# Optimization experiments

Measured on AMD Instinct MI355X. Metric: run time of the kernel, lower is better.

Reference implementation:

```python
import jax, jax.numpy as jnp
import numpy as np

D_G, D_2D, D_3D = 512, 768, 1024
D_F, RANK, ATTN_H = 256, 16, 512
B = 8192


def _xavier(key, shape):
    fan_out, fan_in = shape
    lim = float(np.sqrt(6.0 / (fan_in + fan_out)))
    return jax.random.uniform(key, shape, jnp.float32, -lim, lim)


def setup_inputs() -> dict:
    key = jax.random.key(0)
    ks = jax.random.split(key, 12)
    inp = {
        "h_g": jax.random.normal(ks[0], (B, D_G), jnp.float32),
        "h_2d": jax.random.normal(ks[1], (B, D_2D), jnp.float32),
        "h_3d": jax.random.normal(ks[2], (B, D_3D), jnp.float32),
        # modality projections (torch Linear: y = x @ W.T + b)
        "Wg": _xavier(ks[3], (D_F, D_G)),   "bg": jnp.zeros((D_F,), jnp.float32),
        "W2": _xavier(ks[4], (D_F, D_2D)),  "b2": jnp.zeros((D_F,), jnp.float32),
        "W3": _xavier(ks[5], (D_F, D_3D)),  "b3": jnp.zeros((D_F,), jnp.float32),
        # LayerNorm affine params
        "ln_g_w": jnp.ones((D_F,), jnp.float32),  "ln_g_b": jnp.zeros((D_F,), jnp.float32),
        "ln_2_w": jnp.ones((D_F,), jnp.float32),  "ln_2_b": jnp.zeros((D_F,), jnp.float32),
        "ln_3_w": jnp.ones((D_F,), jnp.float32),  "ln_3_b": jnp.zeros((D_F,), jnp.float32),
        # rank expansions (no bias)
        "U": _xavier(ks[6], (RANK * D_F, D_F)),
        "V": _xavier(ks[7], (RANK * D_F, D_F)),
        "S": _xavier(ks[8], (RANK * D_F, D_F)),
        # attention MLP
        "Wa1": _xavier(ks[9], (ATTN_H, D_G + D_2D + D_3D)), "ba1": jnp.zeros((ATTN_H,), jnp.float32),
        "Wa2": _xavier(ks[10], (RANK, ATTN_H)),             "ba2": jnp.zeros((RANK,), jnp.float32),
    }
    return inp


def _layernorm(x, w, b, eps=1e-5):
    mu = jnp.mean(x, axis=-1, keepdims=True)
    var = jnp.var(x, axis=-1, keepdims=True)
    return (x - mu) * jax.lax.rsqrt(var + eps) * w + b


def reference(h_g, h_2d, h_3d, Wg, bg, W2, b2, W3, b3,
              ln_g_w, ln_g_b, ln_2_w, ln_2_b, ln_3_w, ln_3_b,
              U, V, S, Wa1, ba1, Wa2, ba2):
    # proj + LN + ReLU (dropout=0 / eval mode)
    g = jax.nn.relu(_layernorm(h_g @ Wg.T + bg, ln_g_w, ln_g_b))
    d2 = jax.nn.relu(_layernorm(h_2d @ W2.T + b2, ln_2_w, ln_2_b))
    d3 = jax.nn.relu(_layernorm(h_3d @ W3.T + b3, ln_3_w, ln_3_b))
    b = g.shape[0]
    # rank expansion: (B, R, d_f)
    g_r = (g @ U.T).reshape(b, RANK, D_F)
    d2_r = (d2 @ V.T).reshape(b, RANK, D_F)
    d3_r = (d3 @ S.T).reshape(b, RANK, D_F)
    z_r = g_r * d2_r * d3_r  # elementwise tri-linear product
    # rank attention from raw modality concat
    h_cat = jnp.concatenate([h_g, h_2d, h_3d], axis=-1)
    beta = jax.nn.softmax(jax.nn.relu(h_cat @ Wa1.T + ba1) @ Wa2.T + ba2, axis=-1)  # (B, R)
    z = jnp.einsum('brd,br->bd', z_r, beta)  # (B, d_f)
    return z
```

## Files before the change

### kernel.cpp

```cpp
#include <hip/hip_runtime.h>
#include <stdint.h>

#define B_ROWS 8192
#define DG 512
#define D2 768
#define D3 1024
#define DCAT 2304
#define DF 256
#define RANK 16
#define AH 512

#define OFF_WG 0
#define OFF_W2 131072
#define OFF_W3 327680
#define OFF_U  589824
#define OFF_V  1638400
#define OFF_S  2686976
#define OFF_WA1 3735552

#define WS_WBUF  0u
#define WS_HG    9830400u
#define WS_H2    18219008u
#define WS_H3    30801920u
#define WS_GBUF  47579136u
#define WS_A1P   60162048u
#define WS_ZPART 60162048u
#define WS_BETA  93716480u
#define WS_REQUIRED 94240768u

typedef __attribute__((ext_vector_type(8))) short short8;
typedef __attribute__((ext_vector_type(4))) float f32x4;

__device__ inline unsigned short f2bf(float f) {
  union { float f; unsigned int u; } v; v.f = f;
  unsigned int u = v.u + 0x7fffu + ((v.u >> 16) & 1u);
  return (unsigned short)(u >> 16);
}
__device__ inline float bf2f(unsigned short h) {
  union { float f; unsigned int u; } v; v.u = ((unsigned int)h) << 16;
  return v.f;
}

typedef const unsigned int __attribute__((address_space(1)))* as1_u32p;
typedef unsigned int __attribute__((address_space(3)))* as3_u32p;

__device__ inline void g2l16(const unsigned short* g, unsigned short* l) {
  __builtin_amdgcn_global_load_lds((as1_u32p)g, (as3_u32p)l, 16, 0, 0);
}


__global__ __launch_bounds__(256) void cvt_split_k(const float* __restrict__ hg,
                                                   const float* __restrict__ h2,
                                                   const float* __restrict__ h3,
                                                   const float* __restrict__ Wg,
                                                   const float* __restrict__ W2,
                                                   const float* __restrict__ W3,
                                                   const float* __restrict__ U,
                                                   const float* __restrict__ V,
                                                   const float* __restrict__ S,
                                                   const float* __restrict__ Wa1,
                                                   unsigned short* __restrict__ hgb,
                                                   unsigned short* __restrict__ h2b,
                                                   unsigned short* __restrict__ h3b,
                                                   unsigned short* __restrict__ wbuf) {
  const int bid = blockIdx.x;
  const float* src;
  unsigned short* dst;
  int e;
  if (bid < 18432) {
    e = (bid * 256 + threadIdx.x) * 4;
    if (e < 4194304)        { src = hg + e;            dst = hgb + e; }
    else if (e < 10485760)  { src = h2 + (e - 4194304); dst = h2b + (e - 4194304); }
    else                    { src = h3 + (e - 10485760); dst = h3b + (e - 10485760); }
  } else {
    e = ((bid - 18432) * 256 + threadIdx.x) * 4;
    dst = wbuf + e;
    if (e < OFF_W2)       src = Wg  + e;
    else if (e < OFF_W3)  src = W2  + (e - OFF_W2);
    else if (e < OFF_U)   src = W3  + (e - OFF_W3);
    else if (e < OFF_V)   src = U   + (e - OFF_U);
    else if (e < OFF_S)   src = V   + (e - OFF_V);
    else if (e < OFF_WA1) src = S   + (e - OFF_S);
    else                  src = Wa1 + (e - OFF_WA1);
  }
  float4 v = *(const float4*)src;
  ushort4 o;
  o.x = f2bf(v.x); o.y = f2bf(v.y); o.z = f2bf(v.z); o.w = f2bf(v.w);
  *(ushort4*)dst = o;
}


__global__ __launch_bounds__(512, 2) void fatgemm256_k(const unsigned short* __restrict__ hgb,
                                                       const unsigned short* __restrict__ h2b,
                                                       const unsigned short* __restrict__ h3b,
                                                       const unsigned short* __restrict__ wbuf,
                                                       const float* __restrict__ bg,
                                                       const float* __restrict__ b2,
                                                       const float* __restrict__ b3,
                                                       const float* __restrict__ wg,
                                                       const float* __restrict__ wbg,
                                                       const float* __restrict__ w2,
                                                       const float* __restrict__ wb2,
                                                       const float* __restrict__ w3,
                                                       const float* __restrict__ wb3,
                                                       unsigned short* __restrict__ gout,
                                                       unsigned short* __restrict__ a1part) {
  __shared__ __align__(16) unsigned short lA[2 * 256 * 64];
  __shared__ __align__(16) unsigned short lB[2 * 256 * 64];
  const int bid = blockIdx.x;
  const int tid = threadIdx.x;
  const int lane = tid & 63;
  const int wid = tid >> 6;
  const int wr = wid >> 2;
  const int wc = wid & 3;
  const int row_s = tid >> 3;
  const int kc_s = (((tid & 7) ^ (row_s & 7)) << 3);
  const int mbase = wr * 128 + (lane & 15);
  const int nbase = wc * 64 + (lane & 15);
  const int kq = lane >> 4;
  const int h = lane & 7;

  int role_a1 = 0, half = 0, m0 = 0, n0 = 0, z = 0, nt = 0;
  if (bid < 64)       { role_a1 = 1; half = 0; n0 = (bid & 1) << 8; m0 = (bid >> 1) << 8; nt = 20; }
  else if (bid < 96)  { z = 2; m0 = (bid - 64) << 8; nt = 16; }
  else if (bid < 160) { role_a1 = 1; half = 1; int r6 = bid - 96; n0 = (r6 & 1) << 8; m0 = (r6 >> 1) << 8; nt = 16; }
  else if (bid < 192) { z = 1; m0 = (bid - 160) << 8; nt = 12; }
  else                { z = 0; m0 = (bid - 192) << 8; nt = 8; }

  const unsigned short* projA = (z == 0) ? hgb : ((z == 1) ? h2b : h3b);
  const int Kz   = (z == 0) ? DG : ((z == 1) ? D2 : D3);
  const int woff = (z == 0) ? OFF_WG : ((z == 1) ? OFF_W2 : OFF_W3);

  auto stage = [&](int t, unsigned short* dA, unsigned short* dB) {
    const unsigned short* Ag; int lda; int ka;
    const unsigned short* Bg; int ldb; int kb;
    if (role_a1) {
      const int tt = half ? (20 + t) : t;
      if (tt < 8)       { Ag = hgb; lda = DG; ka = tt * 64; }
      else if (tt < 20) { Ag = h2b; lda = D2; ka = (tt - 8) * 64; }
      else              { Ag = h3b; lda = D3; ka = (tt - 20) * 64; }
      Ag += (size_t)m0 * lda;
      Bg = wbuf + OFF_WA1 + (size_t)n0 * DCAT; ldb = DCAT; kb = tt * 64;
    } else {
      lda = Kz; Ag = projA + (size_t)m0 * lda; ka = t * 64;
      ldb = Kz; Bg = wbuf + woff;              kb = t * 64;
    }
#pragma unroll
    for (int q = 0; q < 4; ++q) {
      const int row = q * 64 + row_s;
      const int lofs = (q * 512 + tid) * 8;
      g2l16(Ag + (size_t)row * lda + ka + kc_s, dA + lofs);
      g2l16(Bg + (size_t)row * ldb + kb + kc_s, dB + lofs);
    }
  };

  f32x4 acc[8][4];
#pragma unroll
  for (int ti = 0; ti < 8; ++ti)
#pragma unroll
    for (int tj = 0; tj < 4; ++tj)
      acc[ti][tj] = (f32x4){0.f, 0.f, 0.f, 0.f};

  auto compute = [&](const unsigned short* sA, const unsigned short* sB) {
#pragma unroll
    for (int kk = 0; kk < 2; ++kk) {
      const int kch = (kk << 2) + kq;
      const int ko = ((kch ^ h) << 3);
      short8 af[8], bfr[4];
#pragma unroll
      for (int t4 = 0; t4 < 8; ++t4)
        af[t4] = *(const short8*)(sA + (mbase + t4 * 16) * 64 + ko);
#pragma unroll
      for (int t4 = 0; t4 < 4; ++t4)
        bfr[t4] = *(const short8*)(sB + (nbase + t4 * 16) * 64 + ko);
      __builtin_amdgcn_s_setprio(1);
#pragma unroll
      for (int ti = 0; ti < 8; ++ti)
#pragma unroll
        for (int tj = 0; tj < 4; ++tj)
          acc[ti][tj] = __builtin_amdgcn_mfma_f32_16x16x32_bf16(af[ti], bfr[tj], acc[ti][tj], 0, 0, 0);
      __builtin_amdgcn_s_setprio(0);
    }
  };

  stage(0, lA, lB);
  stage(1, lA + 16384, lB + 16384);
  for (int t = 0; t < nt; ++t) {
    const int b = t & 1;
    unsigned short* cA = lA + b * 16384;
    unsigned short* cB = lB + b * 16384;
    if (t + 1 < nt) asm volatile("s_waitcnt vmcnt(8)" ::: "memory");
    else            asm volatile("s_waitcnt vmcnt(0)" ::: "memory");
    __builtin_amdgcn_s_barrier();
    __builtin_amdgcn_sched_barrier(0);
    compute(cA, cB);
    __builtin_amdgcn_sched_barrier(0);
    __builtin_amdgcn_s_barrier();
    if (t + 2 < nt) stage(t + 2, cA, cB);
  }

  if (role_a1) {
    unsigned short* out = a1part + (size_t)half * (B_ROWS * AH);
    const int r0 = m0 + wr * 128 + ((lane >> 4) << 2);
    const int c0 = n0 + wc * 64 + (lane & 15);
#pragma unroll
    for (int ti = 0; ti < 8; ++ti)
#pragma unroll
      for (int tj = 0; tj < 4; ++tj)
#pragma unroll
        for (int i = 0; i < 4; ++i)
          out[(size_t)(r0 + ti * 16 + i) * AH + (c0 + tj * 16)] = f2bf(acc[ti][tj][i]);
  } else {
    const float* bias = (z == 0) ? bg : ((z == 1) ? b2 : b3);
    const float* lnw  = (z == 0) ? wg : ((z == 1) ? w2 : w3);
    const float* lnb  = (z == 0) ? wbg : ((z == 1) ? wb2 : wb3);
    const int cbase = wc * 64 + (lane & 15);
    float bs[4], lw4[4], lb4[4];
#pragma unroll
    for (int tj = 0; tj < 4; ++tj) {
      const int col = cbase + tj * 16;
      bs[tj] = bias[col]; lw4[tj] = lnw[col]; lb4[tj] = lnb[col];
    }
#pragma unroll
    for (int ti = 0; ti < 8; ++ti)
#pragma unroll
      for (int tj = 0; tj < 4; ++tj)
#pragma unroll
        for (int i = 0; i < 4; ++i)
          acc[ti][tj][i] += bs[tj];

    float* lnr = (float*)lA;
    __syncthreads();
#pragma unroll
    for (int ti = 0; ti < 8; ++ti)
#pragma unroll
      for (int i = 0; i < 4; ++i) {
        float s = acc[ti][0][i] + acc[ti][1][i] + acc[ti][2][i] + acc[ti][3][i];
        float q = acc[ti][0][i] * acc[ti][0][i] + acc[ti][1][i] * acc[ti][1][i]
                + acc[ti][2][i] * acc[ti][2][i] + acc[ti][3][i] * acc[ti][3][i];
#pragma unroll
        for (int m = 1; m < 16; m <<= 1) { s += __shfl_xor(s, m, 64); q += __shfl_xor(q, m, 64); }
        if ((lane & 15) == 0) {
          const int rl = wr * 128 + ti * 16 + ((lane >> 4) << 2) + i;
          lnr[rl * 8 + wc * 2]     = s;
          lnr[rl * 8 + wc * 2 + 1] = q;
        }
      }
    __syncthreads();
    unsigned short* gz = gout + (size_t)z * (B_ROWS * DF);
#pragma unroll
    for (int ti = 0; ti < 8; ++ti)
#pragma unroll
      for (int i = 0; i < 4; ++i) {
        const int rl = wr * 128 + ti * 16 + ((lane >> 4) << 2) + i;
        const float4 pa = *(const float4*)(lnr + rl * 8);
        const float4 pb = *(const float4*)(lnr + rl * 8 + 4);
        const float sum = pa.x + pa.z + pb.x + pb.z;
        const float sq  = pa.y + pa.w + pb.y + pb.w;
        const float mean = sum * (1.f / DF);
        const float var  = sq * (1.f / DF) - mean * mean;
        const float rs   = rsqrtf(var + 1e-5f);
        const size_t rowoff = (size_t)(m0 + rl) * DF;
#pragma unroll
        for (int tj = 0; tj < 4; ++tj) {
          const float v = (acc[ti][tj][i] - mean) * rs * lw4[tj] + lb4[tj];
          gz[rowoff + cbase + tj * 16] = f2bf(fmaxf(v, 0.f));
        }
      }
  }
}


__global__ __launch_bounds__(256, 2) void rank_fused_k(const unsigned short* __restrict__ gbuf,
                                                       const unsigned short* __restrict__ wbuf,
                                                       const float* __restrict__ beta,
                                                       float* __restrict__ zpart) {
  __shared__ __align__(16) unsigned short lA[2 * 128 * 64];
  __shared__ __align__(16) unsigned short lB[2 * 128 * 64];
  __shared__ float lbeta[4 * 128];
  const int m0 = blockIdx.x * 128;
  const int d0 = blockIdx.y * 128;
  const int rg = blockIdx.z * 4;
  const int tid = threadIdx.x;

  for (int i = tid; i < 512; i += 256) {
    const int rr = i >> 7, row = i & 127;
    lbeta[i] = beta[(size_t)(m0 + row) * RANK + rg + rr];
  }
  __syncthreads();

  const int lane = tid & 63;
  const int wr = tid >> 7, wc = (tid >> 6) & 1;
  const int row_s = tid >> 3;
  const int kc_s = (((tid & 7) ^ ((tid >> 3) & 7)) << 3);
  const int mbase = wr * 64 + (lane & 15);
  const int nbase = wc * 64 + (lane & 15);
  const int kq = lane >> 4;
  const int h = lane & 7;
  const int lr0 = wr * 64 + ((lane >> 4) << 2);

  const unsigned short* Abase = gbuf + (size_t)(m0 + row_s) * DF + kc_s;
  const unsigned short* Bbase = wbuf + OFF_U + (size_t)(rg * 256 + d0 + row_s) * DF + kc_s;

  auto stage = [&](int t, unsigned short* dA, unsigned short* dB) {
    const int p = t >> 2, ks = t & 3;
    const int rr = p / 3;
    const int zi = p - rr * 3;
    const unsigned short* Ag = Abase + (size_t)zi * (B_ROWS * DF) + ks * 64;
    const unsigned short* Bg = Bbase + (size_t)zi * 1048576 + (size_t)rr * (256 * DF) + ks * 64;
#pragma unroll
    for (int q = 0; q < 4; ++q) {
      const int lofs = (q * 256 + tid) * 8;
      g2l16(Ag + (size_t)q * 32 * DF, dA + lofs);
      g2l16(Bg + (size_t)q * 32 * DF, dB + lofs);
    }
  };

  f32x4 zacc[4][4], prod[4][4], acc[4][4];
#pragma unroll
  for (int ti = 0; ti < 4; ++ti)
#pragma unroll
    for (int tj = 0; tj < 4; ++tj) {
      zacc[ti][tj] = (f32x4){0.f, 0.f, 0.f, 0.f};
      acc[ti][tj]  = (f32x4){0.f, 0.f, 0.f, 0.f};
    }

  auto compute = [&](const unsigned short* sA, const unsigned short* sB) {
#pragma unroll
    for (int kk = 0; kk < 2; ++kk) {
      const int kch = (kk << 2) + kq;
      const int ko = ((kch ^ h) << 3);
      short8 af[4], bfr[4];
#pragma unroll
      for (int t4 = 0; t4 < 4; ++t4) {
        af[t4]  = *(const short8*)(sA + (mbase + t4 * 16) * 64 + ko);
        bfr[t4] = *(const short8*)(sB + (nbase + t4 * 16) * 64 + ko);
      }
      __builtin_amdgcn_s_setprio(1);
#pragma unroll
      for (int ti = 0; ti < 4; ++ti)
#pragma unroll
        for (int tj = 0; tj < 4; ++tj)
          acc[ti][tj] = __builtin_amdgcn_mfma_f32_16x16x32_bf16(af[ti], bfr[tj], acc[ti][tj], 0, 0, 0);
      __builtin_amdgcn_s_setprio(0);
    }
  };

  stage(0, lA, lB);
  stage(1, lA + 8192, lB + 8192);

  for (int p = 0; p < 12; ++p) {
    const int rr = p / 3;
    const int zi = p - rr * 3;
#pragma unroll
    for (int ks = 0; ks < 4; ++ks) {
      const int t = (p << 2) + ks;
      const int b = t & 1;
      unsigned short* cA = lA + b * 8192;
      unsigned short* cB = lB + b * 8192;
      if (t < 47) asm volatile("s_waitcnt vmcnt(8)" ::: "memory");
      else        asm volatile("s_waitcnt vmcnt(0)" ::: "memory");
      __builtin_amdgcn_s_barrier();
      __builtin_amdgcn_sched_barrier(0);
      compute(cA, cB);
      __builtin_amdgcn_sched_barrier(0);
      __builtin_amdgcn_s_barrier();
      if (t + 2 < 48) stage(t + 2, cA, cB);
    }

    if (zi == 0) {
#pragma unroll
      for (int ti = 0; ti < 4; ++ti)
#pragma unroll
        for (int tj = 0; tj < 4; ++tj)
          prod[ti][tj] = acc[ti][tj];
    } else if (zi == 1) {
#pragma unroll
      for (int ti = 0; ti < 4; ++ti)
#pragma unroll
        for (int tj = 0; tj < 4; ++tj)
          prod[ti][tj] *= acc[ti][tj];
    } else {
#pragma unroll
      for (int ti = 0; ti < 4; ++ti) {
        const float4 b4 = *(const float4*)(lbeta + rr * 128 + lr0 + ti * 16);
        const float bv[4] = {b4.x, b4.y, b4.z, b4.w};
#pragma unroll
        for (int tj = 0; tj < 4; ++tj)
#pragma unroll
          for (int i = 0; i < 4; ++i)
            zacc[ti][tj][i] += prod[ti][tj][i] * acc[ti][tj][i] * bv[i];
      }
    }
#pragma unroll
    for (int ti = 0; ti < 4; ++ti)
#pragma unroll
      for (int tj = 0; tj < 4; ++tj)
        acc[ti][tj] = (f32x4){0.f, 0.f, 0.f, 0.f};
  }

  float* zp = zpart + (size_t)blockIdx.z * (B_ROWS * DF);
  const int c0 = d0 + wc * 64 + (lane & 15);
#pragma unroll
  for (int ti = 0; ti < 4; ++ti)
#pragma unroll
    for (int tj = 0; tj < 4; ++tj)
#pragma unroll
      for (int i = 0; i < 4; ++i)
        zp[(size_t)(m0 + lr0 + ti * 16 + i) * DF + (c0 + tj * 16)] = zacc[ti][tj][i];
}


__global__ __launch_bounds__(256) void zsum_k(const float* __restrict__ zpart,
                                              float* __restrict__ z) {
  const int idx = blockIdx.x * 256 + threadIdx.x;
  const size_t e = (size_t)idx * 4;
  const size_t stride = (size_t)B_ROWS * DF;
  float4 a = *(const float4*)(zpart + e);
  float4 b = *(const float4*)(zpart + stride + e);
  float4 c = *(const float4*)(zpart + 2 * stride + e);
  float4 d = *(const float4*)(zpart + 3 * stride + e);
  float4 o;
  o.x = (a.x + b.x) + (c.x + d.x);
  o.y = (a.y + b.y) + (c.y + d.y);
  o.z = (a.z + b.z) + (c.z + d.z);
  o.w = (a.w + b.w) + (c.w + d.w);
  *(float4*)(z + e) = o;
}


__global__ __launch_bounds__(256) void post_beta_k(const unsigned short* __restrict__ a1part,
                                                   const float* __restrict__ ba1,
                                                   const float* __restrict__ Wa2,
                                                   const float* __restrict__ ba2,
                                                   float* __restrict__ beta) {
  __shared__ float lw[RANK * AH];
  for (int i = threadIdx.x; i < RANK * AH / 4; i += 256)
    *(float4*)(lw + i * 4) = *(const float4*)(Wa2 + i * 4);
  __syncthreads();
  const int row = blockIdx.x * 4 + (threadIdx.x >> 6);
  const int lane = threadIdx.x & 63;
  const unsigned short* h0 = a1part + (size_t)row * AH + lane * 8;
  const unsigned short* h1 = h0 + (size_t)B_ROWS * AH;
  const uint4 p0 = *(const uint4*)h0;
  const uint4 p1 = *(const uint4*)h1;
  const unsigned int u0[4] = {p0.x, p0.y, p0.z, p0.w};
  const unsigned int u1[4] = {p1.x, p1.y, p1.z, p1.w};
  float4 ca = *(const float4*)(ba1 + lane * 8);
  float4 cb = *(const float4*)(ba1 + lane * 8 + 4);
  const float bias[8] = {ca.x, ca.y, ca.z, ca.w, cb.x, cb.y, cb.z, cb.w};
  float av[8];
#pragma unroll
  for (int j = 0; j < 4; ++j) {
    const float s0 = bf2f((unsigned short)(u0[j] & 0xffffu)) + bf2f((unsigned short)(u1[j] & 0xffffu));
    const float s1 = bf2f((unsigned short)(u0[j] >> 16)) + bf2f((unsigned short)(u1[j] >> 16));
    av[2 * j]     = fmaxf(s0 + bias[2 * j], 0.f);
    av[2 * j + 1] = fmaxf(s1 + bias[2 * j + 1], 0.f);
  }
  float lg[RANK];
#pragma unroll
  for (int r = 0; r < RANK; ++r) {
    const float* wrow = lw + r * AH + lane * 8;
    float4 wa = *(const float4*)wrow;
    float4 wb = *(const float4*)(wrow + 4);
    float p = av[0] * wa.x + av[1] * wa.y + av[2] * wa.z + av[3] * wa.w
            + av[4] * wb.x + av[5] * wb.y + av[6] * wb.z + av[7] * wb.w;
#pragma unroll
    for (int m = 1; m < 64; m <<= 1) p += __shfl_xor(p, m, 64);
    lg[r] = p + ba2[r];
  }
  float mx = lg[0];
#pragma unroll
  for (int r = 1; r < RANK; ++r) mx = fmaxf(mx, lg[r]);
  float den = 0.f;
#pragma unroll
  for (int r = 0; r < RANK; ++r) { lg[r] = __expf(lg[r] - mx); den += lg[r]; }
  const float inv = 1.f / den;
  if (lane < RANK) {
    float mine = 0.f;
#pragma unroll
    for (int r = 0; r < RANK; ++r) mine = (lane == r) ? lg[r] : mine;
    beta[(size_t)row * RANK + lane] = mine * inv;
  }
}


extern "C" void kernel_launch(void* const* d_in, const int* in_sizes, int n_in,
                              void* d_out, int out_size, void* d_ws, size_t ws_size,
                              hipStream_t stream) {
  if (ws_size < (size_t)WS_REQUIRED) return;

  const float* h_g   = (const float*)d_in[0];
  const float* h_2d  = (const float*)d_in[1];
  const float* h_3d  = (const float*)d_in[2];
  const float* Wg    = (const float*)d_in[3];
  const float* bg    = (const float*)d_in[4];
  const float* W2    = (const float*)d_in[5];
  const float* b2    = (const float*)d_in[6];
  const float* W3    = (const float*)d_in[7];
  const float* b3    = (const float*)d_in[8];
  const float* ln_g_w = (const float*)d_in[9];
  const float* ln_g_b = (const float*)d_in[10];
  const float* ln_2_w = (const float*)d_in[11];
  const float* ln_2_b = (const float*)d_in[12];
  const float* ln_3_w = (const float*)d_in[13];
  const float* ln_3_b = (const float*)d_in[14];
  const float* U     = (const float*)d_in[15];
  const float* V     = (const float*)d_in[16];
  const float* S     = (const float*)d_in[17];
  const float* Wa1   = (const float*)d_in[18];
  const float* ba1   = (const float*)d_in[19];
  const float* Wa2   = (const float*)d_in[20];
  const float* ba2   = (const float*)d_in[21];

  char* ws = (char*)d_ws;
  unsigned short* wbuf   = (unsigned short*)(ws + WS_WBUF);
  unsigned short* hgb    = (unsigned short*)(ws + WS_HG);
  unsigned short* h2b    = (unsigned short*)(ws + WS_H2);
  unsigned short* h3b    = (unsigned short*)(ws + WS_H3);
  unsigned short* gbuf   = (unsigned short*)(ws + WS_GBUF);
  unsigned short* a1part = (unsigned short*)(ws + WS_A1P);
  float*          zpart  = (float*)(ws + WS_ZPART);
  float*          beta   = (float*)(ws + WS_BETA);
  float* z = (float*)d_out;

  cvt_split_k<<<dim3(23232), dim3(256), 0, stream>>>(h_g, h_2d, h_3d,
                                                     Wg, W2, W3, U, V, S, Wa1,
                                                     hgb, h2b, h3b, wbuf);
  fatgemm256_k<<<dim3(224), dim3(512), 0, stream>>>(hgb, h2b, h3b, wbuf,
                                                    bg, b2, b3,
                                                    ln_g_w, ln_g_b, ln_2_w, ln_2_b,
                                                    ln_3_w, ln_3_b,
                                                    gbuf, a1part);
  post_beta_k<<<dim3(2048), dim3(256), 0, stream>>>(a1part, ba1, Wa2, ba2, beta);
  rank_fused_k<<<dim3(64, 2, 4), dim3(256), 0, stream>>>(gbuf, wbuf, beta, zpart);
  zsum_k<<<dim3(2048), dim3(256), 0, stream>>>(zpart, z);
}
```

Baseline: 296.5 us.

## Fuse fp32-to-bf16 activation conversion into the GEMM A-tile load path

Drops the separate conversion pass over the three input activation matrices. The fused GEMM now loads fp32 A tiles into registers, converts them to bf16 and writes them to LDS itself, prefetching the next tile while the current one is consumed. B tiles still go through direct global-to-LDS loads. This removes a full write and re-read of the bf16 activation copies, but each GEMM block now reads fp32 activations (twice the bytes) and adds register pressure and conversion ALU work to the main loop, with a changed wait-count schedule.

```diff
diff --git a/kernel.cpp b/kernel.cpp
--- a/kernel.cpp
+++ b/kernel.cpp
@@ -19,13 +19,10 @@
 #define OFF_WA1 3735552
 
 #define WS_WBUF  0u
-#define WS_HG    9830400u
-#define WS_H2    18219008u
-#define WS_H3    30801920u
-#define WS_GBUF  47579136u
-#define WS_A1P   60162048u
-#define WS_ZPART 60162048u
-#define WS_BETA  93716480u
+#define WS_GBUF  9830400u
+#define WS_A1P   22413312u
+#define WS_ZPART 22413312u
+#define WS_BETA  55967744u
 #define WS_REQUIRED 94240768u
 
 typedef __attribute__((ext_vector_type(8))) short short8;
@@ -49,50 +46,33 @@
 }
 
 
-__global__ __launch_bounds__(256) void cvt_split_k(const float* __restrict__ hg,
-                                                   const float* __restrict__ h2,
-                                                   const float* __restrict__ h3,
-                                                   const float* __restrict__ Wg,
-                                                   const float* __restrict__ W2,
-                                                   const float* __restrict__ W3,
-                                                   const float* __restrict__ U,
-                                                   const float* __restrict__ V,
-                                                   const float* __restrict__ S,
-                                                   const float* __restrict__ Wa1,
-                                                   unsigned short* __restrict__ hgb,
-                                                   unsigned short* __restrict__ h2b,
-                                                   unsigned short* __restrict__ h3b,
-                                                   unsigned short* __restrict__ wbuf) {
-  const int bid = blockIdx.x;
+__global__ __launch_bounds__(256) void cvt_w_k(const float* __restrict__ Wg,
+                                               const float* __restrict__ W2,
+                                               const float* __restrict__ W3,
+                                               const float* __restrict__ U,
+                                               const float* __restrict__ V,
+                                               const float* __restrict__ S,
+                                               const float* __restrict__ Wa1,
+                                               unsigned short* __restrict__ wbuf) {
+  const int e = (blockIdx.x * 256 + threadIdx.x) * 4;
   const float* src;
-  unsigned short* dst;
-  int e;
-  if (bid < 18432) {
-    e = (bid * 256 + threadIdx.x) * 4;
-    if (e < 4194304)        { src = hg + e;            dst = hgb + e; }
-    else if (e < 10485760)  { src = h2 + (e - 4194304); dst = h2b + (e - 4194304); }
-    else                    { src = h3 + (e - 10485760); dst = h3b + (e - 10485760); }
-  } else {
-    e = ((bid - 18432) * 256 + threadIdx.x) * 4;
-    dst = wbuf + e;
-    if (e < OFF_W2)       src = Wg  + e;
-    else if (e < OFF_W3)  src = W2  + (e - OFF_W2);
-    else if (e < OFF_U)   src = W3  + (e - OFF_W3);
-    else if (e < OFF_V)   src = U   + (e - OFF_U);
-    else if (e < OFF_S)   src = V   + (e - OFF_V);
-    else if (e < OFF_WA1) src = S   + (e - OFF_S);
-    else                  src = Wa1 + (e - OFF_WA1);
-  }
+  if (e < OFF_W2)       src = Wg  + e;
+  else if (e < OFF_W3)  src = W2  + (e - OFF_W2);
+  else if (e < OFF_U)   src = W3  + (e - OFF_W3);
+  else if (e < OFF_V)   src = U   + (e - OFF_U);
+  else if (e < OFF_S)   src = V   + (e - OFF_V);
+  else if (e < OFF_WA1) src = S   + (e - OFF_S);
+  else                  src = Wa1 + (e - OFF_WA1);
   float4 v = *(const float4*)src;
   ushort4 o;
   o.x = f2bf(v.x); o.y = f2bf(v.y); o.z = f2bf(v.z); o.w = f2bf(v.w);
-  *(ushort4*)dst = o;
-}
-
-
-__global__ __launch_bounds__(512, 2) void fatgemm256_k(const unsigned short* __restrict__ hgb,
-                                                       const unsigned short* __restrict__ h2b,
-                                                       const unsigned short* __restrict__ h3b,
+  *(ushort4*)(wbuf + e) = o;
+}
+
+
+__global__ __launch_bounds__(512, 2) void fatgemm256_k(const float* __restrict__ hgf,
+                                                       const float* __restrict__ h2f,
+                                                       const float* __restrict__ h3f,
                                                        const unsigned short* __restrict__ wbuf,
                                                        const float* __restrict__ bg,
                                                        const float* __restrict__ b2,
@@ -127,31 +107,54 @@
   else if (bid < 192) { z = 1; m0 = (bid - 160) << 8; nt = 12; }
   else                { z = 0; m0 = (bid - 192) << 8; nt = 8; }
 
-  const unsigned short* projA = (z == 0) ? hgb : ((z == 1) ? h2b : h3b);
+  const float* projA = (z == 0) ? hgf : ((z == 1) ? h2f : h3f);
   const int Kz   = (z == 0) ? DG : ((z == 1) ? D2 : D3);
   const int woff = (z == 0) ? OFF_WG : ((z == 1) ? OFF_W2 : OFF_W3);
 
-  auto stage = [&](int t, unsigned short* dA, unsigned short* dB) {
-    const unsigned short* Ag; int lda; int ka;
+  float4 ar[8];
+  auto loadA = [&](int t) {
+    const float* Ag; int lda; int ka;
+    if (role_a1) {
+      const int tt = half ? (20 + t) : t;
+      if (tt < 8)       { Ag = hgf; lda = DG; ka = tt * 64; }
+      else if (tt < 20) { Ag = h2f; lda = D2; ka = (tt - 8) * 64; }
+      else              { Ag = h3f; lda = D3; ka = (tt - 20) * 64; }
+      Ag += (size_t)m0 * lda;
+    } else {
+      lda = Kz; Ag = projA + (size_t)m0 * lda; ka = t * 64;
+    }
+#pragma unroll
+    for (int q = 0; q < 4; ++q) {
+      const float* src = Ag + (size_t)(q * 64 + row_s) * lda + ka + kc_s;
+      ar[q * 2]     = *(const float4*)src;
+      ar[q * 2 + 1] = *(const float4*)(src + 4);
+    }
+  };
+
+  auto writeA = [&](unsigned short* dA) {
+#pragma unroll
+    for (int q = 0; q < 4; ++q) {
+      const float4 a = ar[q * 2], b = ar[q * 2 + 1];
+      short8 w;
+      w[0] = (short)f2bf(a.x); w[1] = (short)f2bf(a.y);
+      w[2] = (short)f2bf(a.z); w[3] = (short)f2bf(a.w);
+      w[4] = (short)f2bf(b.x); w[5] = (short)f2bf(b.y);
+      w[6] = (short)f2bf(b.z); w[7] = (short)f2bf(b.w);
+      *(short8*)(dA + (q * 512 + tid) * 8) = w;
+    }
+  };
+
+  auto stageB = [&](int t, unsigned short* dB) {
     const unsigned short* Bg; int ldb; int kb;
     if (role_a1) {
       const int tt = half ? (20 + t) : t;
-      if (tt < 8)       { Ag = hgb; lda = DG; ka = tt * 64; }
-      else if (tt < 20) { Ag = h2b; lda = D2; ka = (tt - 8) * 64; }
-      else              { Ag = h3b; lda = D3; ka = (tt - 20) * 64; }
-      Ag += (size_t)m0 * lda;
       Bg = wbuf + OFF_WA1 + (size_t)n0 * DCAT; ldb = DCAT; kb = tt * 64;
     } else {
-      lda = Kz; Ag = projA + (size_t)m0 * lda; ka = t * 64;
-      ldb = Kz; Bg = wbuf + woff;              kb = t * 64;
-    }
-#pragma unroll
-    for (int q = 0; q < 4; ++q) {
-      const int row = q * 64 + row_s;
-      const int lofs = (q * 512 + tid) * 8;
-      g2l16(Ag + (size_t)row * lda + ka + kc_s, dA + lofs);
-      g2l16(Bg + (size_t)row * ldb + kb + kc_s, dB + lofs);
-    }
+      Bg = wbuf + woff; ldb = Kz; kb = t * 64;
+    }
+#pragma unroll
+    for (int q = 0; q < 4; ++q)
+      g2l16(Bg + (size_t)(q * 64 + row_s) * ldb + kb + kc_s, dB + (q * 512 + tid) * 8);
   };
 
   f32x4 acc[8][4];
@@ -183,20 +186,26 @@
     }
   };
 
-  stage(0, lA, lB);
-  stage(1, lA + 16384, lB + 16384);
+  stageB(0, lB);
+  loadA(0);
+  stageB(1, lB + 16384);
+
   for (int t = 0; t < nt; ++t) {
     const int b = t & 1;
     unsigned short* cA = lA + b * 16384;
     unsigned short* cB = lB + b * 16384;
-    if (t + 1 < nt) asm volatile("s_waitcnt vmcnt(8)" ::: "memory");
+    if (t + 1 < nt) asm volatile("s_waitcnt vmcnt(4)" ::: "memory");
     else            asm volatile("s_waitcnt vmcnt(0)" ::: "memory");
+    __builtin_amdgcn_sched_barrier(0);
+    writeA(cA);
+    if (t + 1 < nt) loadA(t + 1);
+    asm volatile("s_waitcnt lgkmcnt(0)" ::: "memory");
     __builtin_amdgcn_s_barrier();
     __builtin_amdgcn_sched_barrier(0);
     compute(cA, cB);
     __builtin_amdgcn_sched_barrier(0);
     __builtin_amdgcn_s_barrier();
-    if (t + 2 < nt) stage(t + 2, cA, cB);
+    if (t + 2 < nt) stageB(t + 2, cB);
   }
 
   if (role_a1) {
@@ -515,19 +524,14 @@
 
   char* ws = (char*)d_ws;
   unsigned short* wbuf   = (unsigned short*)(ws + WS_WBUF);
-  unsigned short* hgb    = (unsigned short*)(ws + WS_HG);
-  unsigned short* h2b    = (unsigned short*)(ws + WS_H2);
-  unsigned short* h3b    = (unsigned short*)(ws + WS_H3);
   unsigned short* gbuf   = (unsigned short*)(ws + WS_GBUF);
   unsigned short* a1part = (unsigned short*)(ws + WS_A1P);
   float*          zpart  = (float*)(ws + WS_ZPART);
   float*          beta   = (float*)(ws + WS_BETA);
   float* z = (float*)d_out;
 
-  cvt_split_k<<<dim3(23232), dim3(256), 0, stream>>>(h_g, h_2d, h_3d,
-                                                     Wg, W2, W3, U, V, S, Wa1,
-                                                     hgb, h2b, h3b, wbuf);
-  fatgemm256_k<<<dim3(224), dim3(512), 0, stream>>>(hgb, h2b, h3b, wbuf,
+  cvt_w_k<<<dim3(4800), dim3(256), 0, stream>>>(Wg, W2, W3, U, V, S, Wa1, wbuf);
+  fatgemm256_k<<<dim3(224), dim3(512), 0, stream>>>(h_g, h_2d, h_3d, wbuf,
                                                     bg, b2, b3,
                                                     ln_g_w, ln_g_b, ln_2_w, ln_2_b,
                                                     ln_3_w, ln_3_b,
```

Result: faster. 287.3 us (-3.1%).
